# Optimization experiments

Measured on AMD Instinct MI355X. Metric: run time of the kernel, lower is better.

Reference implementation:

```python
import jax, jax.numpy as jnp
import numpy as np

BN_EPS = 1e-5

def _deg_inv_sqrt(idx, n):
    deg = jax.ops.segment_sum(jnp.ones(idx.shape, jnp.float32), idx, num_segments=n)
    return jnp.where(deg > 0, 1.0 / jnp.sqrt(jnp.maximum(deg, 1.0)), 0.0)

def setup_inputs() -> dict:
    key = jax.random.key(0)
    ks = jax.random.split(key, 8)
    N, E, D, L = 50000, 500000, 128, 3
    node_ids = jax.random.randint(ks[0], (N,), 0, 343)
    src = jax.random.randint(ks[1], (E,), 0, N, dtype=jnp.int32)
    dst = jax.random.randint(ks[2], (E,), 0, N, dtype=jnp.int32)
    emb_table = jax.random.normal(ks[3], (343, D), jnp.float32)
    s = 1.0 / np.sqrt(D)
    Ws = jax.random.normal(ks[4], (L, D, D), jnp.float32) * s
    bs = jnp.zeros((L, D), jnp.float32)
    Rws = jax.random.normal(ks[5], (L, D, D), jnp.float32) * s
    Rbs = jnp.zeros((L, D), jnp.float32)
    gammas = jnp.ones((L, D), jnp.float32)
    betas = jnp.zeros((L, D), jnp.float32)
    return dict(node_ids=node_ids, src=src, dst=dst, emb_table=emb_table,
                Ws=Ws, bs=bs, Rws=Rws, Rbs=Rbs, gammas=gammas, betas=betas)

def reference(node_ids, src, dst, emb_table, Ws, bs, Rws, Rbs, gammas, betas):
    N = node_ids.shape[0]
    L = Ws.shape[0]
    # GraphConv norm='both': src side uses out-degree, dst side uses in-degree
    out_norm = _deg_inv_sqrt(src, N)  # [N]
    in_norm = _deg_inv_sqrt(dst, N)   # [N]
    x = emb_table[node_ids]           # [N, D] embedding lookup
    for l in range(L):
        # D^{-1/2} A D^{-1/2} X, then linear + bias + activation (DGL GraphConv)
        h = x * out_norm[:, None]
        agg = jax.ops.segment_sum(h[src], dst, num_segments=N) * in_norm[:, None]
        h = jax.nn.relu(agg @ Ws[l] + bs[l])
        # residual branch: activation(Linear(x)) added (dgllife GCNLayer)
        h = h + jax.nn.relu(x @ Rws[l] + Rbs[l])
        # dropout p=0 (identity), then BatchNorm1d (batch statistics)
        mu = h.mean(axis=0)
        var = h.var(axis=0)
        x = gammas[l] * (h - mu) / jnp.sqrt(var + BN_EPS) + betas[l]
    return x
```

## Files before the change

### kernel.cpp

```cpp
#include <hip/hip_runtime.h>
#include <hip/hip_bf16.h>


#define TPB 256
#define NBANK 8
#define GM 16
#define APAD 136

typedef __attribute__((ext_vector_type(8))) short bf16x8;
typedef __attribute__((ext_vector_type(4))) float f32x4;

__device__ inline unsigned short f2bf(float f) {
    unsigned int u = __builtin_bit_cast(unsigned int, f);
    u += 0x7fff + ((u >> 16) & 1);
    return (unsigned short)(u >> 16);
}
__device__ inline float bf2f(unsigned short b) {
    unsigned int u = ((unsigned int)b) << 16;
    return __builtin_bit_cast(float, u);
}


__global__ void degree_kernel(const int* __restrict__ src, const int* __restrict__ dst,
                              int* __restrict__ deg_src, int* __restrict__ deg_dst,
                              int* __restrict__ rank, int e) {
    int i = blockIdx.x * blockDim.x + threadIdx.x;
    if (i < e) {
        atomicAdd(&deg_src[src[i]], 1);
        rank[i] = atomicAdd(&deg_dst[dst[i]], 1);
    }
}

__global__ void scan1_norm(const int* __restrict__ deg_src, const int* __restrict__ deg_dst,
                           float* __restrict__ out_norm, float* __restrict__ in_norm,
                           int* __restrict__ row_ptr, int* __restrict__ bsum, int n) {
    __shared__ int tmp[1024];
    int t = threadIdx.x;
    int i = blockIdx.x * 1024 + t;
    int v = (i < n) ? deg_dst[i] : 0;
    tmp[t] = v;
    __syncthreads();
    for (int off = 1; off < 1024; off <<= 1) {
        int add = (t >= off) ? tmp[t - off] : 0;
        __syncthreads();
        tmp[t] += add;
        __syncthreads();
    }
    if (i < n) {
        row_ptr[i] = tmp[t] - v;
        int dsv = deg_src[i];
        out_norm[i] = dsv > 0 ? rsqrtf((float)dsv) : 0.f;
        in_norm[i]  = v   > 0 ? rsqrtf((float)v)   : 0.f;
    }
    if (t == 1023) bsum[blockIdx.x] = tmp[1023];
}

__global__ void scan_apply(const int* __restrict__ bsum, int* __restrict__ row_ptr,
                           int n, int e) {
    __shared__ int boff;
    if (threadIdx.x == 0) {
        int r = 0;
        for (int b2 = 0; b2 < blockIdx.x; b2++) r += bsum[b2];
        boff = r;
    }
    __syncthreads();
    int i = blockIdx.x * 1024 + threadIdx.x;
    if (i < n) row_ptr[i] += boff;
    if (i == n) row_ptr[n] = e;
}

__global__ void scatter_kernel(const int* __restrict__ src, const int* __restrict__ dst,
                               const int* __restrict__ row_ptr, const int* __restrict__ rank,
                               const float* __restrict__ out_norm,
                               int2* __restrict__ col_un, int e) {
    int i = blockIdx.x * blockDim.x + threadIdx.x;
    if (i < e) {
        int s = src[i];
        int2 v;
        v.x = s;
        v.y = __float_as_int(out_norm[s]);
        col_un[row_ptr[dst[i]] + rank[i]] = v;
    }
}

__global__ void embed_prep(const int* __restrict__ node_ids, const float* __restrict__ emb,
                           unsigned short* __restrict__ x, int n32,
                           const float* __restrict__ Ws, const float* __restrict__ Rws,
                           unsigned short* __restrict__ Wt, unsigned short* __restrict__ Rwt,
                           int wtotal) {
    int gid = blockIdx.x * blockDim.x + threadIdx.x;
    if (gid < n32) {
        int v = gid >> 5, c4 = gid & 31;
        int id = node_ids[v];
        float4 e = *(const float4*)&emb[id * 128 + c4 * 4];
        ushort4 o;
        o.x = f2bf(e.x); o.y = f2bf(e.y); o.z = f2bf(e.z); o.w = f2bf(e.w);
        *(ushort4*)&x[(size_t)v * 128 + c4 * 4] = o;
    }
    if (gid < wtotal) {
        int l = gid >> 14, r = (gid >> 7) & 127, k = gid & 127;
        int sidx = l * 16384 + k * 128 + r;
        Wt[gid]  = f2bf(Ws[sidx]);
        Rwt[gid] = f2bf(Rws[sidx]);
    }
}

__global__ __launch_bounds__(256, 6) void fused_layer_kernel(
    const unsigned short* __restrict__ x,
    const int* __restrict__ row_ptr, const int2* __restrict__ col_un,
    const float* __restrict__ in_norm,
    const unsigned short* __restrict__ Wt, const unsigned short* __restrict__ Rwt,
    const float* __restrict__ bvec, const float* __restrict__ Rbvec,
    float* __restrict__ h, float* __restrict__ stats, int nrows) {
    __shared__ unsigned short As[GM * APAD];
    __shared__ unsigned short Xs[GM * APAD];
    __shared__ float bsum[128], bss[128];
    int tid = threadIdx.x;
    int m0 = blockIdx.x * GM;
    if (tid < 128) { bsum[tid] = 0.f; bss[tid] = 0.f; }

    {
        int node = tid >> 4;
        int part = tid & 15;
        int gnode = m0 + node;
        if (gnode >= nrows) gnode = nrows - 1;
        uint4 xv = *(const uint4*)&x[(size_t)gnode * 128 + part * 8];
        *(uint4*)&Xs[node * APAD + part * 8] = xv;
        float inv = in_norm[gnode];
        int beg = row_ptr[gnode], end = row_ptr[gnode + 1];
        float acc[8];
        #pragma unroll
        for (int j = 0; j < 8; j++) acc[j] = 0.f;
        const unsigned short* xb = x + part * 8;
        for (int e = beg; e < end; e += 8) {
            int rem = end - e;
            int2 ed[8];
            #pragma unroll
            for (int j = 0; j < 8; j++) ed[j] = col_un[e + j];
            uint4 q[8];
            #pragma unroll
            for (int j = 0; j < 8; j++)
                q[j] = *(const uint4*)(xb + (size_t)(unsigned)ed[j].x * 128);
            #pragma unroll
            for (int j = 0; j < 8; j++) {
                float nn = (j < rem) ? __int_as_float(ed[j].y) : 0.f;
                const unsigned int* w = (const unsigned int*)&q[j];
                #pragma unroll
                for (int t = 0; t < 4; t++) {
                    acc[2 * t]     += nn * bf2f((unsigned short)w[t]);
                    acc[2 * t + 1] += nn * bf2f((unsigned short)(w[t] >> 16));
                }
            }
        }
        #pragma unroll
        for (int j = 0; j < 8; j++) acc[j] *= inv;
        uint4 pk;
        pk.x = (unsigned int)f2bf(acc[0]) | ((unsigned int)f2bf(acc[1]) << 16);
        pk.y = (unsigned int)f2bf(acc[2]) | ((unsigned int)f2bf(acc[3]) << 16);
        pk.z = (unsigned int)f2bf(acc[4]) | ((unsigned int)f2bf(acc[5]) << 16);
        pk.w = (unsigned int)f2bf(acc[6]) | ((unsigned int)f2bf(acc[7]) << 16);
        *(uint4*)&As[node * APAD + part * 8] = pk;
    }
    __syncthreads();

    int wave = tid >> 6;
    int lane = tid & 63;
    int m = lane & 15;
    int quad = lane >> 4;

    f32x4 accA[2], accX[2];
    #pragma unroll
    for (int t = 0; t < 2; t++) { accA[t] = (f32x4){0,0,0,0}; accX[t] = (f32x4){0,0,0,0}; }

    #pragma unroll
    for (int kc = 0; kc < 4; kc++) {
        int koff = kc * 32 + quad * 8;
        bf16x8 aA = *(const bf16x8*)&As[m * APAD + koff];
        bf16x8 aX = *(const bf16x8*)&Xs[m * APAD + koff];
        #pragma unroll
        for (int t = 0; t < 2; t++) {
            int nrow = (wave * 2 + t) * 16 + m;
            bf16x8 bW = *(const bf16x8*)&Wt[(size_t)nrow * 128 + koff];
            bf16x8 bR = *(const bf16x8*)&Rwt[(size_t)nrow * 128 + koff];
            accA[t] = __builtin_amdgcn_mfma_f32_16x16x32_bf16(aA, bW, accA[t], 0, 0, 0);
            accX[t] = __builtin_amdgcn_mfma_f32_16x16x32_bf16(aX, bR, accX[t], 0, 0, 0);
        }
    }

    #pragma unroll
    for (int t = 0; t < 2; t++) {
        int col = (wave * 2 + t) * 16 + m;
        float bW = bvec[col], bR = Rbvec[col];
        float cs = 0.f, cq = 0.f;
        #pragma unroll
        for (int reg = 0; reg < 4; reg++) {
            int gr = m0 + quad * 4 + reg;
            float hA = accA[t][reg] + bW; hA = hA > 0.f ? hA : 0.f;
            float hX = accX[t][reg] + bR; hX = hX > 0.f ? hX : 0.f;
            float v = hA + hX;
            if (gr < nrows) {
                h[(size_t)gr * 128 + col] = v;
            } else {
                v = 0.f;
            }
            cs += v; cq += v * v;
        }
        cs += __shfl_xor(cs, 16); cs += __shfl_xor(cs, 32);
        cq += __shfl_xor(cq, 16); cq += __shfl_xor(cq, 32);
        if (lane < 16) {
            atomicAdd(&bsum[col], cs);
            atomicAdd(&bss[col], cq);
        }
    }
    __syncthreads();
    if (tid < 128) {
        float* sb = stats + (size_t)(blockIdx.x & (NBANK - 1)) * 256;
        atomicAdd(&sb[tid], bsum[tid]);
        atomicAdd(&sb[tid + 128], bss[tid]);
    }
}


__global__ void norm_apply_bf16(const float* __restrict__ h, const float* __restrict__ stats,
                                const float* __restrict__ gamma, const float* __restrict__ beta,
                                unsigned short* __restrict__ dstp, int total4, float n) {
    __shared__ float ssc[128], ssh[128];
    int t = threadIdx.x;
    if (t < 128) {
        float s = 0.f, sq = 0.f;
        #pragma unroll
        for (int b2 = 0; b2 < NBANK; b2++) {
            s  += stats[b2 * 256 + t];
            sq += stats[b2 * 256 + t + 128];
        }
        float mu = s / n;
        float var = sq / n - mu * mu;
        float rstd = rsqrtf(var + 1e-5f);
        float sc = gamma[t] * rstd;
        ssc[t] = sc;
        ssh[t] = beta[t] - sc * mu;
    }
    __syncthreads();
    int gid = blockIdx.x * blockDim.x + t;
    if (gid >= total4) return;
    int c4 = gid & 31;
    float4 sc = *(const float4*)&ssc[c4 * 4];
    float4 sh = *(const float4*)&ssh[c4 * 4];
    float4 v = ((const float4*)h)[gid];
    ushort4 o;
    o.x = f2bf(sc.x * v.x + sh.x);
    o.y = f2bf(sc.y * v.y + sh.y);
    o.z = f2bf(sc.z * v.z + sh.z);
    o.w = f2bf(sc.w * v.w + sh.w);
    ((ushort4*)dstp)[gid] = o;
}

__global__ void norm_apply_f32(const float* __restrict__ h, const float* __restrict__ stats,
                               const float* __restrict__ gamma, const float* __restrict__ beta,
                               float* __restrict__ dstp, int total4, float n) {
    __shared__ float ssc[128], ssh[128];
    int t = threadIdx.x;
    if (t < 128) {
        float s = 0.f, sq = 0.f;
        #pragma unroll
        for (int b2 = 0; b2 < NBANK; b2++) {
            s  += stats[b2 * 256 + t];
            sq += stats[b2 * 256 + t + 128];
        }
        float mu = s / n;
        float var = sq / n - mu * mu;
        float rstd = rsqrtf(var + 1e-5f);
        float sc = gamma[t] * rstd;
        ssc[t] = sc;
        ssh[t] = beta[t] - sc * mu;
    }
    __syncthreads();
    int gid = blockIdx.x * blockDim.x + t;
    if (gid >= total4) return;
    int c4 = gid & 31;
    float4 sc = *(const float4*)&ssc[c4 * 4];
    float4 sh = *(const float4*)&ssh[c4 * 4];
    float4 v = ((const float4*)h)[gid];
    float4 o;
    o.x = sc.x * v.x + sh.x;
    o.y = sc.y * v.y + sh.y;
    o.z = sc.z * v.z + sh.z;
    o.w = sc.w * v.w + sh.w;
    ((float4*)dstp)[gid] = o;
}


extern "C" void kernel_launch(void* const* d_in, const int* in_sizes, int n_in,
                              void* d_out, int out_size, void* d_ws, size_t ws_size,
                              hipStream_t stream) {
    const int*   node_ids = (const int*)d_in[0];
    const int*   src      = (const int*)d_in[1];
    const int*   dst      = (const int*)d_in[2];
    const float* emb      = (const float*)d_in[3];
    const float* Ws       = (const float*)d_in[4];
    const float* bs       = (const float*)d_in[5];
    const float* Rws      = (const float*)d_in[6];
    const float* Rbs      = (const float*)d_in[7];
    const float* gammas   = (const float*)d_in[8];
    const float* betas    = (const float*)d_in[9];

    const int N = in_sizes[0];
    const int E = in_sizes[1];
    const int D = 128;
    const int L = in_sizes[4] / (D * D);

    size_t off = 0;
    auto alloc = [&](size_t bytes) -> void* {
        void* p = (char*)d_ws + off;
        off += (bytes + 255) & ~(size_t)255;
        return p;
    };
    int*   degs     = (int*)alloc((size_t)2 * N * 4);
    int*   deg_src  = degs;
    int*   deg_dst  = degs + N;
    int*   rank     = (int*)alloc((size_t)E * 4);
    float* out_norm = (float*)alloc((size_t)N * 4);
    float* in_norm  = (float*)alloc((size_t)N * 4);
    int*   row_ptr  = (int*)alloc((size_t)(N + 1) * 4);
    int*   bsumg    = (int*)alloc(64 * 4);
    int2*  col_un   = (int2*)alloc(((size_t)E + 8) * 8);
    float* stats    = (float*)alloc((size_t)L * NBANK * 256 * 4);
    unsigned short* Wt  = (unsigned short*)alloc((size_t)L * D * D * 2);
    unsigned short* Rwt = (unsigned short*)alloc((size_t)L * D * D * 2);
    unsigned short* x   = (unsigned short*)alloc((size_t)N * D * 2);
    float* h = (float*)d_out;

    hipMemsetAsync(degs, 0, (size_t)2 * N * 4, stream);
    hipMemsetAsync(stats, 0, (size_t)L * NBANK * 256 * 4, stream);
    hipMemsetAsync(col_un + E, 0, 8 * sizeof(int2), stream);

    degree_kernel<<<(E + TPB - 1) / TPB, TPB, 0, stream>>>(src, dst, deg_src, deg_dst, rank, E);
    int nb = (N + 1023) / 1024;
    scan1_norm<<<nb, 1024, 0, stream>>>(deg_src, deg_dst, out_norm, in_norm, row_ptr, bsumg, N);
    scan_apply<<<nb, 1024, 0, stream>>>(bsumg, row_ptr, N, E);
    scatter_kernel<<<(E + TPB - 1) / TPB, TPB, 0, stream>>>(src, dst, row_ptr, rank,
                                                            out_norm, col_un, E);
    int n32 = N * 32, wtotal = L * D * D;
    int epg = ((n32 > wtotal ? n32 : wtotal) + TPB - 1) / TPB;
    embed_prep<<<epg, TPB, 0, stream>>>(node_ids, emb, x, n32, Ws, Rws, Wt, Rwt, wtotal);

    int gblocks = (N + GM - 1) / GM;
    for (int l = 0; l < L; l++) {
        const unsigned short* Wtl  = Wt  + (size_t)l * D * D;
        const unsigned short* Rwtl = Rwt + (size_t)l * D * D;
        const float* b   = bs  + (size_t)l * D;
        const float* Rb  = Rbs + (size_t)l * D;
        const float* gm  = gammas + (size_t)l * D;
        const float* bt  = betas  + (size_t)l * D;
        float* st = stats + (size_t)l * NBANK * 256;

        fused_layer_kernel<<<gblocks, TPB, 0, stream>>>(
            x, row_ptr, col_un, in_norm, Wtl, Rwtl, b, Rb, h, st, N);
        if (l < L - 1) {
            norm_apply_bf16<<<(N * 32 + TPB - 1) / TPB, TPB, 0, stream>>>(
                h, st, gm, bt, x, N * 32, (float)N);
        } else {
            norm_apply_f32<<<(N * 32 + TPB - 1) / TPB, TPB, 0, stream>>>(
                h, st, gm, bt, (float*)d_out, N * 32, (float)N);
        }
    }
}
```

Baseline: 313.5 us.

## Fold BatchNorm into next layer's gather and replicate degree counters

The intermediate BatchNorm apply kernels are removed. The previous layer's normalization is applied inside the next fused layer kernel as a per-column scale and shift, using a running sum of edge norms for the aggregated term. Intermediate activations are now written as bf16 through shared memory, where fp32 was written before. Degree counting uses 8 replicated counter arrays to reduce atomic contention, is merged with the embedding prep kernel, and processes 4 edges per thread. Risks include extra bf16 rounding of the pre-norm activations and a larger memset for the replicated counters.

```diff
diff --git a/kernel.cpp b/kernel.cpp
--- a/kernel.cpp
+++ b/kernel.cpp
@@ -6,6 +6,7 @@
 #define NBANK 8
 #define GM 16
 #define APAD 136
+#define NREP 8
 
 typedef __attribute__((ext_vector_type(8))) short bf16x8;
 typedef __attribute__((ext_vector_type(4))) float f32x4;
@@ -20,24 +21,78 @@
     return __builtin_bit_cast(float, u);
 }
 
-
-__global__ void degree_kernel(const int* __restrict__ src, const int* __restrict__ dst,
-                              int* __restrict__ deg_src, int* __restrict__ deg_dst,
-                              int* __restrict__ rank, int e) {
-    int i = blockIdx.x * blockDim.x + threadIdx.x;
-    if (i < e) {
-        atomicAdd(&deg_src[src[i]], 1);
-        rank[i] = atomicAdd(&deg_dst[dst[i]], 1);
-    }
-}
-
-__global__ void scan1_norm(const int* __restrict__ deg_src, const int* __restrict__ deg_dst,
+__global__ void prep1(const int* __restrict__ node_ids, const float* __restrict__ emb,
+                      unsigned short* __restrict__ x, int n32,
+                      const float* __restrict__ Ws, const float* __restrict__ Rws,
+                      unsigned short* __restrict__ Wt, unsigned short* __restrict__ Rwt,
+                      int wtotal,
+                      const int* __restrict__ src, const int* __restrict__ dst,
+                      int* __restrict__ deg_rep, int* __restrict__ rank,
+                      int E, int N, int degBlocks) {
+    if ((int)blockIdx.x < degBlocks) {
+        int rep = blockIdx.x & (NREP - 1);
+        int* ds = deg_rep + rep * 2 * N;
+        int* dd = ds + N;
+        int T = degBlocks * 256;
+        int t0 = blockIdx.x * 256 + threadIdx.x;
+        int idx[4], sv[4], dv[4];
+        #pragma unroll
+        for (int k = 0; k < 4; k++) {
+            int i = t0 + k * T;
+            idx[k] = (i < E) ? i : 0;
+        }
+        #pragma unroll
+        for (int k = 0; k < 4; k++) { sv[k] = src[idx[k]]; dv[k] = dst[idx[k]]; }
+        #pragma unroll
+        for (int k = 0; k < 4; k++)
+            if (t0 + k * T < E) atomicAdd(&ds[sv[k]], 1);
+        int r[4];
+        #pragma unroll
+        for (int k = 0; k < 4; k++)
+            r[k] = (t0 + k * T < E) ? atomicAdd(&dd[dv[k]], 1) : 0;
+        #pragma unroll
+        for (int k = 0; k < 4; k++)
+            if (t0 + k * T < E) rank[t0 + k * T] = r[k] | (rep << 24);
+    } else {
+        int gid = (blockIdx.x - degBlocks) * 256 + threadIdx.x;
+        if (gid < n32) {
+            int v = gid >> 5, c4 = gid & 31;
+            int id = node_ids[v];
+            float4 e = *(const float4*)&emb[id * 128 + c4 * 4];
+            ushort4 o;
+            o.x = f2bf(e.x); o.y = f2bf(e.y); o.z = f2bf(e.z); o.w = f2bf(e.w);
+            *(ushort4*)&x[(size_t)v * 128 + c4 * 4] = o;
+        }
+        if (gid < wtotal) {
+            int l = gid >> 14, rr = (gid >> 7) & 127, k = gid & 127;
+            int sidx = l * 16384 + k * 128 + rr;
+            Wt[gid]  = f2bf(Ws[sidx]);
+            Rwt[gid] = f2bf(Rws[sidx]);
+        }
+    }
+}
+
+__global__ void scan1_norm(int* __restrict__ deg_rep,
                            float* __restrict__ out_norm, float* __restrict__ in_norm,
                            int* __restrict__ row_ptr, int* __restrict__ bsum, int n) {
     __shared__ int tmp[1024];
     int t = threadIdx.x;
     int i = blockIdx.x * 1024 + t;
-    int v = (i < n) ? deg_dst[i] : 0;
+    int v = 0;
+    if (i < n) {
+        int dsv = 0, run = 0;
+        #pragma unroll
+        for (int r = 0; r < NREP; r++) {
+            int* base = deg_rep + r * 2 * n;
+            dsv += base[i];
+            int c = base[n + i];
+            base[n + i] = run;
+            run += c;
+        }
+        v = run;
+        out_norm[i] = dsv > 0 ? rsqrtf((float)dsv) : 0.f;
+        in_norm[i]  = v   > 0 ? rsqrtf((float)v)   : 0.f;
+    }
     tmp[t] = v;
     __syncthreads();
     for (int off = 1; off < 1024; off <<= 1) {
@@ -46,12 +101,7 @@
         tmp[t] += add;
         __syncthreads();
     }
-    if (i < n) {
-        row_ptr[i] = tmp[t] - v;
-        int dsv = deg_src[i];
-        out_norm[i] = dsv > 0 ? rsqrtf((float)dsv) : 0.f;
-        in_norm[i]  = v   > 0 ? rsqrtf((float)v)   : 0.f;
-    }
+    if (i < n) row_ptr[i] = tmp[t] - v;
     if (t == 1023) bsum[blockIdx.x] = tmp[1023];
 }
 
@@ -60,7 +110,7 @@
     __shared__ int boff;
     if (threadIdx.x == 0) {
         int r = 0;
-        for (int b2 = 0; b2 < blockIdx.x; b2++) r += bsum[b2];
+        for (int b2 = 0; b2 < (int)blockIdx.x; b2++) r += bsum[b2];
         boff = r;
     }
     __syncthreads();
@@ -72,66 +122,95 @@
 __global__ void scatter_kernel(const int* __restrict__ src, const int* __restrict__ dst,
                                const int* __restrict__ row_ptr, const int* __restrict__ rank,
                                const float* __restrict__ out_norm,
-                               int2* __restrict__ col_un, int e) {
-    int i = blockIdx.x * blockDim.x + threadIdx.x;
-    if (i < e) {
-        int s = src[i];
-        int2 v;
-        v.x = s;
-        v.y = __float_as_int(out_norm[s]);
-        col_un[row_ptr[dst[i]] + rank[i]] = v;
-    }
-}
-
-__global__ void embed_prep(const int* __restrict__ node_ids, const float* __restrict__ emb,
-                           unsigned short* __restrict__ x, int n32,
-                           const float* __restrict__ Ws, const float* __restrict__ Rws,
-                           unsigned short* __restrict__ Wt, unsigned short* __restrict__ Rwt,
-                           int wtotal) {
-    int gid = blockIdx.x * blockDim.x + threadIdx.x;
-    if (gid < n32) {
-        int v = gid >> 5, c4 = gid & 31;
-        int id = node_ids[v];
-        float4 e = *(const float4*)&emb[id * 128 + c4 * 4];
-        ushort4 o;
-        o.x = f2bf(e.x); o.y = f2bf(e.y); o.z = f2bf(e.z); o.w = f2bf(e.w);
-        *(ushort4*)&x[(size_t)v * 128 + c4 * 4] = o;
-    }
-    if (gid < wtotal) {
-        int l = gid >> 14, r = (gid >> 7) & 127, k = gid & 127;
-        int sidx = l * 16384 + k * 128 + r;
-        Wt[gid]  = f2bf(Ws[sidx]);
-        Rwt[gid] = f2bf(Rws[sidx]);
+                               const int* __restrict__ deg_rep,
+                               int2* __restrict__ col_un, int E, int N, int T) {
+    int t0 = blockIdx.x * blockDim.x + threadIdx.x;
+    int idx[4], sv[4], dv[4], rk[4];
+    #pragma unroll
+    for (int k = 0; k < 4; k++) {
+        int i = t0 + k * T;
+        idx[k] = (i < E) ? i : 0;
+    }
+    #pragma unroll
+    for (int k = 0; k < 4; k++) { sv[k] = src[idx[k]]; dv[k] = dst[idx[k]]; rk[k] = rank[idx[k]]; }
+    int pos[4]; float nm[4];
+    #pragma unroll
+    for (int k = 0; k < 4; k++) {
+        int rep = ((unsigned)rk[k]) >> 24;
+        int lr = rk[k] & 0xFFFFFF;
+        pos[k] = row_ptr[dv[k]] + deg_rep[rep * 2 * N + N + dv[k]] + lr;
+        nm[k] = out_norm[sv[k]];
+    }
+    #pragma unroll
+    for (int k = 0; k < 4; k++) {
+        if (t0 + k * T < E) {
+            int2 v; v.x = sv[k]; v.y = __float_as_int(nm[k]);
+            col_un[pos[k]] = v;
+        }
     }
 }
 
 __global__ __launch_bounds__(256, 6) void fused_layer_kernel(
-    const unsigned short* __restrict__ x,
+    const unsigned short* __restrict__ xin,
     const int* __restrict__ row_ptr, const int2* __restrict__ col_un,
     const float* __restrict__ in_norm,
     const unsigned short* __restrict__ Wt, const unsigned short* __restrict__ Rwt,
     const float* __restrict__ bvec, const float* __restrict__ Rbvec,
-    float* __restrict__ h, float* __restrict__ stats, int nrows) {
+    const float* __restrict__ pstats, const float* __restrict__ pgamma,
+    const float* __restrict__ pbeta, int first, float fN,
+    unsigned short* __restrict__ hout16, float* __restrict__ hout32,
+    float* __restrict__ stats, int nrows) {
     __shared__ unsigned short As[GM * APAD];
     __shared__ unsigned short Xs[GM * APAD];
-    __shared__ float bsum[128], bss[128];
+    __shared__ float bsum[128], bss[128], ssc[128], ssh[128];
     int tid = threadIdx.x;
     int m0 = blockIdx.x * GM;
-    if (tid < 128) { bsum[tid] = 0.f; bss[tid] = 0.f; }
+    if (tid < 128) {
+        float sc = 1.f, sh = 0.f;
+        if (!first) {
+            float s = 0.f, sq = 0.f;
+            #pragma unroll
+            for (int b2 = 0; b2 < NBANK; b2++) {
+                s  += pstats[b2 * 256 + tid];
+                sq += pstats[b2 * 256 + tid + 128];
+            }
+            float mu = s / fN;
+            float var = sq / fN - mu * mu;
+            float rstd = rsqrtf(var + 1e-5f);
+            sc = pgamma[tid] * rstd;
+            sh = pbeta[tid] - sc * mu;
+        }
+        ssc[tid] = sc; ssh[tid] = sh;
+        bsum[tid] = 0.f; bss[tid] = 0.f;
+    }
+    __syncthreads();
 
     {
         int node = tid >> 4;
         int part = tid & 15;
         int gnode = m0 + node;
         if (gnode >= nrows) gnode = nrows - 1;
-        uint4 xv = *(const uint4*)&x[(size_t)gnode * 128 + part * 8];
-        *(uint4*)&Xs[node * APAD + part * 8] = xv;
+        int c0 = part * 8;
+        {
+            uint4 xv = *(const uint4*)&xin[(size_t)gnode * 128 + c0];
+            const unsigned int* w = (const unsigned int*)&xv;
+            uint4 o;
+            unsigned int* op = (unsigned int*)&o;
+            #pragma unroll
+            for (int t2 = 0; t2 < 4; t2++) {
+                float lo = ssc[c0 + 2*t2]     * bf2f((unsigned short)w[t2])         + ssh[c0 + 2*t2];
+                float hi = ssc[c0 + 2*t2 + 1] * bf2f((unsigned short)(w[t2] >> 16)) + ssh[c0 + 2*t2 + 1];
+                op[t2] = (unsigned int)f2bf(lo) | ((unsigned int)f2bf(hi) << 16);
+            }
+            *(uint4*)&Xs[node * APAD + c0] = o;
+        }
         float inv = in_norm[gnode];
         int beg = row_ptr[gnode], end = row_ptr[gnode + 1];
         float acc[8];
+        float snn = 0.f;
         #pragma unroll
         for (int j = 0; j < 8; j++) acc[j] = 0.f;
-        const unsigned short* xb = x + part * 8;
+        const unsigned short* xb = xin + c0;
         for (int e = beg; e < end; e += 8) {
             int rem = end - e;
             int2 ed[8];
@@ -144,6 +223,7 @@
             #pragma unroll
             for (int j = 0; j < 8; j++) {
                 float nn = (j < rem) ? __int_as_float(ed[j].y) : 0.f;
+                snn += nn;
                 const unsigned int* w = (const unsigned int*)&q[j];
                 #pragma unroll
                 for (int t = 0; t < 4; t++) {
@@ -152,14 +232,15 @@
                 }
             }
         }
-        #pragma unroll
-        for (int j = 0; j < 8; j++) acc[j] *= inv;
         uint4 pk;
-        pk.x = (unsigned int)f2bf(acc[0]) | ((unsigned int)f2bf(acc[1]) << 16);
-        pk.y = (unsigned int)f2bf(acc[2]) | ((unsigned int)f2bf(acc[3]) << 16);
-        pk.z = (unsigned int)f2bf(acc[4]) | ((unsigned int)f2bf(acc[5]) << 16);
-        pk.w = (unsigned int)f2bf(acc[6]) | ((unsigned int)f2bf(acc[7]) << 16);
-        *(uint4*)&As[node * APAD + part * 8] = pk;
+        unsigned int* pp = (unsigned int*)&pk;
+        #pragma unroll
+        for (int t2 = 0; t2 < 4; t2++) {
+            float lo = inv * (ssc[c0 + 2*t2]     * acc[2*t2]     + snn * ssh[c0 + 2*t2]);
+            float hi = inv * (ssc[c0 + 2*t2 + 1] * acc[2*t2 + 1] + snn * ssh[c0 + 2*t2 + 1]);
+            pp[t2] = (unsigned int)f2bf(lo) | ((unsigned int)f2bf(hi) << 16);
+        }
+        *(uint4*)&As[node * APAD + c0] = pk;
     }
     __syncthreads();
 
@@ -187,6 +268,7 @@
         }
     }
 
+    float vv[2][4];
     #pragma unroll
     for (int t = 0; t < 2; t++) {
         int col = (wave * 2 + t) * 16 + m;
@@ -197,12 +279,8 @@
             int gr = m0 + quad * 4 + reg;
             float hA = accA[t][reg] + bW; hA = hA > 0.f ? hA : 0.f;
             float hX = accX[t][reg] + bR; hX = hX > 0.f ? hX : 0.f;
-            float v = hA + hX;
-            if (gr < nrows) {
-                h[(size_t)gr * 128 + col] = v;
-            } else {
-                v = 0.f;
-            }
+            float v = (gr < nrows) ? (hA + hX) : 0.f;
+            vv[t][reg] = v;
             cs += v; cq += v * v;
         }
         cs += __shfl_xor(cs, 16); cs += __shfl_xor(cs, 32);
@@ -218,41 +296,31 @@
         atomicAdd(&sb[tid], bsum[tid]);
         atomicAdd(&sb[tid + 128], bss[tid]);
     }
-}
-
-
-__global__ void norm_apply_bf16(const float* __restrict__ h, const float* __restrict__ stats,
-                                const float* __restrict__ gamma, const float* __restrict__ beta,
-                                unsigned short* __restrict__ dstp, int total4, float n) {
-    __shared__ float ssc[128], ssh[128];
-    int t = threadIdx.x;
-    if (t < 128) {
-        float s = 0.f, sq = 0.f;
-        #pragma unroll
-        for (int b2 = 0; b2 < NBANK; b2++) {
-            s  += stats[b2 * 256 + t];
-            sq += stats[b2 * 256 + t + 128];
-        }
-        float mu = s / n;
-        float var = sq / n - mu * mu;
-        float rstd = rsqrtf(var + 1e-5f);
-        float sc = gamma[t] * rstd;
-        ssc[t] = sc;
-        ssh[t] = beta[t] - sc * mu;
-    }
-    __syncthreads();
-    int gid = blockIdx.x * blockDim.x + t;
-    if (gid >= total4) return;
-    int c4 = gid & 31;
-    float4 sc = *(const float4*)&ssc[c4 * 4];
-    float4 sh = *(const float4*)&ssh[c4 * 4];
-    float4 v = ((const float4*)h)[gid];
-    ushort4 o;
-    o.x = f2bf(sc.x * v.x + sh.x);
-    o.y = f2bf(sc.y * v.y + sh.y);
-    o.z = f2bf(sc.z * v.z + sh.z);
-    o.w = f2bf(sc.w * v.w + sh.w);
-    ((ushort4*)dstp)[gid] = o;
+    if (hout32) {
+        #pragma unroll
+        for (int t = 0; t < 2; t++) {
+            int col = (wave * 2 + t) * 16 + m;
+            #pragma unroll
+            for (int reg = 0; reg < 4; reg++) {
+                int gr = m0 + quad * 4 + reg;
+                if (gr < nrows) hout32[(size_t)gr * 128 + col] = vv[t][reg];
+            }
+        }
+    } else {
+        unsigned short* Hs = As;
+        #pragma unroll
+        for (int t = 0; t < 2; t++) {
+            int col = (wave * 2 + t) * 16 + m;
+            #pragma unroll
+            for (int reg = 0; reg < 4; reg++)
+                Hs[(quad * 4 + reg) * 128 + col] = f2bf(vv[t][reg]);
+        }
+        __syncthreads();
+        int r = tid >> 4, c16 = tid & 15;
+        int gr = m0 + r;
+        if (gr < nrows)
+            *(uint4*)&hout16[(size_t)gr * 128 + c16 * 8] = *(const uint4*)&Hs[r * 128 + c16 * 8];
+    }
 }
 
 __global__ void norm_apply_f32(const float* __restrict__ h, const float* __restrict__ stats,
@@ -315,9 +383,7 @@
         off += (bytes + 255) & ~(size_t)255;
         return p;
     };
-    int*   degs     = (int*)alloc((size_t)2 * N * 4);
-    int*   deg_src  = degs;
-    int*   deg_dst  = degs + N;
+    int*   deg_rep  = (int*)alloc((size_t)NREP * 2 * N * 4);
     int*   rank     = (int*)alloc((size_t)E * 4);
     float* out_norm = (float*)alloc((size_t)N * 4);
     float* in_norm  = (float*)alloc((size_t)N * 4);
@@ -328,21 +394,25 @@
     unsigned short* Wt  = (unsigned short*)alloc((size_t)L * D * D * 2);
     unsigned short* Rwt = (unsigned short*)alloc((size_t)L * D * D * 2);
     unsigned short* x   = (unsigned short*)alloc((size_t)N * D * 2);
-    float* h = (float*)d_out;
-
-    hipMemsetAsync(degs, 0, (size_t)2 * N * 4, stream);
+    unsigned short* hb  = (unsigned short*)alloc((size_t)N * D * 2);
+
+    hipMemsetAsync(deg_rep, 0, (size_t)NREP * 2 * N * 4, stream);
     hipMemsetAsync(stats, 0, (size_t)L * NBANK * 256 * 4, stream);
     hipMemsetAsync(col_un + E, 0, 8 * sizeof(int2), stream);
 
-    degree_kernel<<<(E + TPB - 1) / TPB, TPB, 0, stream>>>(src, dst, deg_src, deg_dst, rank, E);
+    int degBlocks = (E + 1023) / 1024;
+    int n32 = N * 32, wtotal = L * D * D;
+    int embBlocks = (n32 + TPB - 1) / TPB;
+    prep1<<<degBlocks + embBlocks, TPB, 0, stream>>>(
+        node_ids, emb, x, n32, Ws, Rws, Wt, Rwt, wtotal,
+        src, dst, deg_rep, rank, E, N, degBlocks);
+
     int nb = (N + 1023) / 1024;
-    scan1_norm<<<nb, 1024, 0, stream>>>(deg_src, deg_dst, out_norm, in_norm, row_ptr, bsumg, N);
+    scan1_norm<<<nb, 1024, 0, stream>>>(deg_rep, out_norm, in_norm, row_ptr, bsumg, N);
     scan_apply<<<nb, 1024, 0, stream>>>(bsumg, row_ptr, N, E);
-    scatter_kernel<<<(E + TPB - 1) / TPB, TPB, 0, stream>>>(src, dst, row_ptr, rank,
-                                                            out_norm, col_un, E);
-    int n32 = N * 32, wtotal = L * D * D;
-    int epg = ((n32 > wtotal ? n32 : wtotal) + TPB - 1) / TPB;
-    embed_prep<<<epg, TPB, 0, stream>>>(node_ids, emb, x, n32, Ws, Rws, Wt, Rwt, wtotal);
+    int scatBlocks = (E + 1023) / 1024;
+    scatter_kernel<<<scatBlocks, TPB, 0, stream>>>(src, dst, row_ptr, rank, out_norm,
+                                                   deg_rep, col_un, E, N, scatBlocks * 256);
 
     int gblocks = (N + GM - 1) / GM;
     for (int l = 0; l < L; l++) {
@@ -350,18 +420,22 @@
         const unsigned short* Rwtl = Rwt + (size_t)l * D * D;
         const float* b   = bs  + (size_t)l * D;
         const float* Rb  = Rbs + (size_t)l * D;
-        const float* gm  = gammas + (size_t)l * D;
-        const float* bt  = betas  + (size_t)l * D;
         float* st = stats + (size_t)l * NBANK * 256;
+        const float* pst = (l > 0) ? stats + (size_t)(l - 1) * NBANK * 256 : stats;
+        const float* pgm = (l > 0) ? gammas + (size_t)(l - 1) * D : gammas;
+        const float* pbt = (l > 0) ? betas  + (size_t)(l - 1) * D : betas;
+
+        const unsigned short* in16 = (l == 1) ? hb : x;
+        unsigned short* out16 = (l == 0) ? hb : ((l == 1) ? x : nullptr);
+        float* out32 = (l == L - 1) ? (float*)d_out : nullptr;
 
         fused_layer_kernel<<<gblocks, TPB, 0, stream>>>(
-            x, row_ptr, col_un, in_norm, Wtl, Rwtl, b, Rb, h, st, N);
-        if (l < L - 1) {
-            norm_apply_bf16<<<(N * 32 + TPB - 1) / TPB, TPB, 0, stream>>>(
-                h, st, gm, bt, x, N * 32, (float)N);
-        } else {
-            norm_apply_f32<<<(N * 32 + TPB - 1) / TPB, TPB, 0, stream>>>(
-                h, st, gm, bt, (float*)d_out, N * 32, (float)N);
-        }
-    }
-}
+            in16, row_ptr, col_un, in_norm, Wtl, Rwtl, b, Rb,
+            pst, pgm, pbt, (l == 0) ? 1 : 0, (float)N,
+            out16, out32, st, N);
+    }
+    norm_apply_f32<<<(N * 32 + TPB - 1) / TPB, TPB, 0, stream>>>(
+        (float*)d_out, stats + (size_t)(L - 1) * NBANK * 256,
+        gammas + (size_t)(L - 1) * D, betas + (size_t)(L - 1) * D,
+        (float*)d_out, N * 32, (float)N);
+}
```

After: 419.2 us. 1.34x slower.

## Replicate degree counters, merge prep kernels, and defer block offsets to consumers

Applied to the files above, without the earlier changes.

Degree counting now spreads atomics over NREP replicated counter arrays and runs in the same launch as the embedding/weight conversion, with each thread handling four edges. The second scan pass is replaced by a single-thread block-offset kernel. Consumers (scatter and the layer kernel) add the block offset and per-replica prefix themselves, which removes a launch and a memset. In exchange there is a larger counter memset, a strided loop in scan1, and extra index loads in the hot layer kernel.

```diff
diff --git a/kernel.cpp b/kernel.cpp
--- a/kernel.cpp
+++ b/kernel.cpp
@@ -6,6 +6,7 @@
 #define NBANK 8
 #define GM 16
 #define APAD 136
+#define NREP 8
 
 typedef __attribute__((ext_vector_type(8))) short bf16x8;
 typedef __attribute__((ext_vector_type(4))) float f32x4;
@@ -20,24 +21,78 @@
     return __builtin_bit_cast(float, u);
 }
 
-
-__global__ void degree_kernel(const int* __restrict__ src, const int* __restrict__ dst,
-                              int* __restrict__ deg_src, int* __restrict__ deg_dst,
-                              int* __restrict__ rank, int e) {
-    int i = blockIdx.x * blockDim.x + threadIdx.x;
-    if (i < e) {
-        atomicAdd(&deg_src[src[i]], 1);
-        rank[i] = atomicAdd(&deg_dst[dst[i]], 1);
-    }
-}
-
-__global__ void scan1_norm(const int* __restrict__ deg_src, const int* __restrict__ deg_dst,
+__global__ void prep1(const int* __restrict__ node_ids, const float* __restrict__ emb,
+                      unsigned short* __restrict__ x, int n32,
+                      const float* __restrict__ Ws, const float* __restrict__ Rws,
+                      unsigned short* __restrict__ Wt, unsigned short* __restrict__ Rwt,
+                      int wtotal,
+                      const int* __restrict__ src, const int* __restrict__ dst,
+                      int* __restrict__ deg_rep, int* __restrict__ rank,
+                      int E, int N, int degBlocks) {
+    if ((int)blockIdx.x < degBlocks) {
+        int rep = blockIdx.x & (NREP - 1);
+        int* ds = deg_rep + rep * 2 * N;
+        int* dd = ds + N;
+        int T = degBlocks * 256;
+        int t0 = blockIdx.x * 256 + threadIdx.x;
+        int idx[4], sv[4], dv[4];
+        #pragma unroll
+        for (int k = 0; k < 4; k++) {
+            int i = t0 + k * T;
+            idx[k] = (i < E) ? i : 0;
+        }
+        #pragma unroll
+        for (int k = 0; k < 4; k++) { sv[k] = src[idx[k]]; dv[k] = dst[idx[k]]; }
+        #pragma unroll
+        for (int k = 0; k < 4; k++)
+            if (t0 + k * T < E) atomicAdd(&ds[sv[k]], 1);
+        int r[4];
+        #pragma unroll
+        for (int k = 0; k < 4; k++)
+            r[k] = (t0 + k * T < E) ? atomicAdd(&dd[dv[k]], 1) : 0;
+        #pragma unroll
+        for (int k = 0; k < 4; k++)
+            if (t0 + k * T < E) rank[t0 + k * T] = r[k] | (rep << 24);
+    } else {
+        int gid = (blockIdx.x - degBlocks) * 256 + threadIdx.x;
+        if (gid < n32) {
+            int v = gid >> 5, c4 = gid & 31;
+            int id = node_ids[v];
+            float4 e = *(const float4*)&emb[id * 128 + c4 * 4];
+            ushort4 o;
+            o.x = f2bf(e.x); o.y = f2bf(e.y); o.z = f2bf(e.z); o.w = f2bf(e.w);
+            *(ushort4*)&x[(size_t)v * 128 + c4 * 4] = o;
+        }
+        if (gid < wtotal) {
+            int l = gid >> 14, rr = (gid >> 7) & 127, k = gid & 127;
+            int sidx = l * 16384 + k * 128 + rr;
+            Wt[gid]  = f2bf(Ws[sidx]);
+            Rwt[gid] = f2bf(Rws[sidx]);
+        }
+    }
+}
+
+__global__ void scan1_norm(int* __restrict__ deg_rep,
                            float* __restrict__ out_norm, float* __restrict__ in_norm,
                            int* __restrict__ row_ptr, int* __restrict__ bsum, int n) {
     __shared__ int tmp[1024];
     int t = threadIdx.x;
     int i = blockIdx.x * 1024 + t;
-    int v = (i < n) ? deg_dst[i] : 0;
+    int v = 0;
+    if (i < n) {
+        int dsv = 0, run = 0;
+        #pragma unroll
+        for (int r = 0; r < NREP; r++) {
+            int* base = deg_rep + r * 2 * n;
+            dsv += base[i];
+            int c = base[n + i];
+            base[n + i] = run;
+            run += c;
+        }
+        v = run;
+        out_norm[i] = dsv > 0 ? rsqrtf((float)dsv) : 0.f;
+        in_norm[i]  = v   > 0 ? rsqrtf((float)v)   : 0.f;
+    }
     tmp[t] = v;
     __syncthreads();
     for (int off = 1; off < 1024; off <<= 1) {
@@ -46,72 +101,59 @@
         tmp[t] += add;
         __syncthreads();
     }
-    if (i < n) {
-        row_ptr[i] = tmp[t] - v;
-        int dsv = deg_src[i];
-        out_norm[i] = dsv > 0 ? rsqrtf((float)dsv) : 0.f;
-        in_norm[i]  = v   > 0 ? rsqrtf((float)v)   : 0.f;
-    }
+    if (i < n) row_ptr[i] = tmp[t] - v;
     if (t == 1023) bsum[blockIdx.x] = tmp[1023];
 }
 
-__global__ void scan_apply(const int* __restrict__ bsum, int* __restrict__ row_ptr,
-                           int n, int e) {
-    __shared__ int boff;
+__global__ void boff_scan(const int* __restrict__ bsum, int* __restrict__ boff, int nb,
+                          int2* __restrict__ col_un_pad) {
     if (threadIdx.x == 0) {
-        int r = 0;
-        for (int b2 = 0; b2 < blockIdx.x; b2++) r += bsum[b2];
-        boff = r;
-    }
-    __syncthreads();
-    int i = blockIdx.x * 1024 + threadIdx.x;
-    if (i < n) row_ptr[i] += boff;
-    if (i == n) row_ptr[n] = e;
+        int run = 0;
+        for (int i = 0; i < nb; i++) { boff[i] = run; run += bsum[i]; }
+    }
+    if (threadIdx.x < 8) { int2 z; z.x = 0; z.y = 0; col_un_pad[threadIdx.x] = z; }
 }
 
 __global__ void scatter_kernel(const int* __restrict__ src, const int* __restrict__ dst,
-                               const int* __restrict__ row_ptr, const int* __restrict__ rank,
+                               const int* __restrict__ row_ptr, const int* __restrict__ boff,
+                               const int* __restrict__ rank,
                                const float* __restrict__ out_norm,
-                               int2* __restrict__ col_un, int e) {
-    int i = blockIdx.x * blockDim.x + threadIdx.x;
-    if (i < e) {
-        int s = src[i];
-        int2 v;
-        v.x = s;
-        v.y = __float_as_int(out_norm[s]);
-        col_un[row_ptr[dst[i]] + rank[i]] = v;
-    }
-}
-
-__global__ void embed_prep(const int* __restrict__ node_ids, const float* __restrict__ emb,
-                           unsigned short* __restrict__ x, int n32,
-                           const float* __restrict__ Ws, const float* __restrict__ Rws,
-                           unsigned short* __restrict__ Wt, unsigned short* __restrict__ Rwt,
-                           int wtotal) {
-    int gid = blockIdx.x * blockDim.x + threadIdx.x;
-    if (gid < n32) {
-        int v = gid >> 5, c4 = gid & 31;
-        int id = node_ids[v];
-        float4 e = *(const float4*)&emb[id * 128 + c4 * 4];
-        ushort4 o;
-        o.x = f2bf(e.x); o.y = f2bf(e.y); o.z = f2bf(e.z); o.w = f2bf(e.w);
-        *(ushort4*)&x[(size_t)v * 128 + c4 * 4] = o;
-    }
-    if (gid < wtotal) {
-        int l = gid >> 14, r = (gid >> 7) & 127, k = gid & 127;
-        int sidx = l * 16384 + k * 128 + r;
-        Wt[gid]  = f2bf(Ws[sidx]);
-        Rwt[gid] = f2bf(Rws[sidx]);
+                               const int* __restrict__ deg_rep,
+                               int2* __restrict__ col_un, int E, int N, int T) {
+    int t0 = blockIdx.x * blockDim.x + threadIdx.x;
+    int idx[4], sv[4], dv[4], rk[4];
+    #pragma unroll
+    for (int k = 0; k < 4; k++) {
+        int i = t0 + k * T;
+        idx[k] = (i < E) ? i : 0;
+    }
+    #pragma unroll
+    for (int k = 0; k < 4; k++) { sv[k] = src[idx[k]]; dv[k] = dst[idx[k]]; rk[k] = rank[idx[k]]; }
+    int pos[4]; float nm[4];
+    #pragma unroll
+    for (int k = 0; k < 4; k++) {
+        int rep = ((unsigned)rk[k]) >> 24;
+        int lr = rk[k] & 0xFFFFFF;
+        pos[k] = row_ptr[dv[k]] + boff[dv[k] >> 10] + deg_rep[rep * 2 * N + N + dv[k]] + lr;
+        nm[k] = out_norm[sv[k]];
+    }
+    #pragma unroll
+    for (int k = 0; k < 4; k++) {
+        if (t0 + k * T < E) {
+            int2 v; v.x = sv[k]; v.y = __float_as_int(nm[k]);
+            col_un[pos[k]] = v;
+        }
     }
 }
 
 __global__ __launch_bounds__(256, 6) void fused_layer_kernel(
     const unsigned short* __restrict__ x,
-    const int* __restrict__ row_ptr, const int2* __restrict__ col_un,
+    const int* __restrict__ row_ptr, const int* __restrict__ boff,
+    const int2* __restrict__ col_un,
     const float* __restrict__ in_norm,
     const unsigned short* __restrict__ Wt, const unsigned short* __restrict__ Rwt,
     const float* __restrict__ bvec, const float* __restrict__ Rbvec,
-    float* __restrict__ h, float* __restrict__ stats, int nrows) {
+    float* __restrict__ h, float* __restrict__ stats, int nrows, int Etot) {
     __shared__ unsigned short As[GM * APAD];
     __shared__ unsigned short Xs[GM * APAD];
     __shared__ float bsum[128], bss[128];
@@ -127,7 +169,9 @@
         uint4 xv = *(const uint4*)&x[(size_t)gnode * 128 + part * 8];
         *(uint4*)&Xs[node * APAD + part * 8] = xv;
         float inv = in_norm[gnode];
-        int beg = row_ptr[gnode], end = row_ptr[gnode + 1];
+        int beg = row_ptr[gnode] + boff[gnode >> 10];
+        int end = (gnode == nrows - 1) ? Etot
+                                       : row_ptr[gnode + 1] + boff[(gnode + 1) >> 10];
         float acc[8];
         #pragma unroll
         for (int j = 0; j < 8; j++) acc[j] = 0.f;
@@ -315,14 +359,13 @@
         off += (bytes + 255) & ~(size_t)255;
         return p;
     };
-    int*   degs     = (int*)alloc((size_t)2 * N * 4);
-    int*   deg_src  = degs;
-    int*   deg_dst  = degs + N;
+    int*   deg_rep  = (int*)alloc((size_t)NREP * 2 * N * 4);
     int*   rank     = (int*)alloc((size_t)E * 4);
     float* out_norm = (float*)alloc((size_t)N * 4);
     float* in_norm  = (float*)alloc((size_t)N * 4);
     int*   row_ptr  = (int*)alloc((size_t)(N + 1) * 4);
     int*   bsumg    = (int*)alloc(64 * 4);
+    int*   boffg    = (int*)alloc(64 * 4);
     int2*  col_un   = (int2*)alloc(((size_t)E + 8) * 8);
     float* stats    = (float*)alloc((size_t)L * NBANK * 256 * 4);
     unsigned short* Wt  = (unsigned short*)alloc((size_t)L * D * D * 2);
@@ -330,19 +373,22 @@
     unsigned short* x   = (unsigned short*)alloc((size_t)N * D * 2);
     float* h = (float*)d_out;
 
-    hipMemsetAsync(degs, 0, (size_t)2 * N * 4, stream);
+    hipMemsetAsync(deg_rep, 0, (size_t)NREP * 2 * N * 4, stream);
     hipMemsetAsync(stats, 0, (size_t)L * NBANK * 256 * 4, stream);
-    hipMemsetAsync(col_un + E, 0, 8 * sizeof(int2), stream);
-
-    degree_kernel<<<(E + TPB - 1) / TPB, TPB, 0, stream>>>(src, dst, deg_src, deg_dst, rank, E);
+
+    int degBlocks = (E + 1023) / 1024;
+    int n32 = N * 32, wtotal = L * D * D;
+    int embBlocks = (n32 + TPB - 1) / TPB;
+    prep1<<<degBlocks + embBlocks, TPB, 0, stream>>>(
+        node_ids, emb, x, n32, Ws, Rws, Wt, Rwt, wtotal,
+        src, dst, deg_rep, rank, E, N, degBlocks);
+
     int nb = (N + 1023) / 1024;
-    scan1_norm<<<nb, 1024, 0, stream>>>(deg_src, deg_dst, out_norm, in_norm, row_ptr, bsumg, N);
-    scan_apply<<<nb, 1024, 0, stream>>>(bsumg, row_ptr, N, E);
-    scatter_kernel<<<(E + TPB - 1) / TPB, TPB, 0, stream>>>(src, dst, row_ptr, rank,
-                                                            out_norm, col_un, E);
-    int n32 = N * 32, wtotal = L * D * D;
-    int epg = ((n32 > wtotal ? n32 : wtotal) + TPB - 1) / TPB;
-    embed_prep<<<epg, TPB, 0, stream>>>(node_ids, emb, x, n32, Ws, Rws, Wt, Rwt, wtotal);
+    scan1_norm<<<nb, 1024, 0, stream>>>(deg_rep, out_norm, in_norm, row_ptr, bsumg, N);
+    boff_scan<<<1, 64, 0, stream>>>(bsumg, boffg, nb, col_un + E);
+    int scatBlocks = (E + 1023) / 1024;
+    scatter_kernel<<<scatBlocks, TPB, 0, stream>>>(src, dst, row_ptr, boffg, rank, out_norm,
+                                                   deg_rep, col_un, E, N, scatBlocks * 256);
 
     int gblocks = (N + GM - 1) / GM;
     for (int l = 0; l < L; l++) {
@@ -355,7 +401,7 @@
         float* st = stats + (size_t)l * NBANK * 256;
 
         fused_layer_kernel<<<gblocks, TPB, 0, stream>>>(
-            x, row_ptr, col_un, in_norm, Wtl, Rwtl, b, Rb, h, st, N);
+            x, row_ptr, boffg, col_un, in_norm, Wtl, Rwtl, b, Rb, h, st, N, E);
         if (l < L - 1) {
             norm_apply_bf16<<<(N * 32 + TPB - 1) / TPB, TPB, 0, stream>>>(
                 h, st, gm, bt, x, N * 32, (float)N);
```

Result: no change. 313.2 us (-0.1%).
